# Kernel tuning notes

Measured on AMD Instinct MI355X. Metric: run time of the kernel, lower is better.

## Reference

```python
import jax, jax.numpy as jnp
import numpy as np
import math

B, T, C = 1, 4096, 1024
N_HEAD = 16
HEAD_DIM = C // N_HEAD


def _rotate_every_two(x):
    x1 = x[..., ::2]
    x2 = x[..., 1::2]
    return jnp.stack((-x2, x1), axis=-1).reshape(x.shape)


def setup_inputs() -> dict:
    key = jax.random.key(0)
    k1, k2, k3 = jax.random.split(key, 3)
    s = 0.02
    return {
        "x": jax.random.normal(k1, (B, T, C), dtype=jnp.float32),
        "Wqkv": jax.random.normal(k2, (C, 3 * C), dtype=jnp.float32) * s,
        "bqkv": jnp.zeros((3 * C,), dtype=jnp.float32),
        "Wproj": jax.random.normal(k3, (C, C), dtype=jnp.float32) * s,
        "bproj": jnp.zeros((C,), dtype=jnp.float32),
    }


def reference(x, Wqkv, bqkv, Wproj, bproj):
    b, t, c = x.shape
    qkv = x @ Wqkv + bqkv                      # [B,T,3C]
    q, k, v = jnp.split(qkv, 3, axis=2)
    # [B,H,T,D]
    q = q.reshape(b, t, N_HEAD, HEAD_DIM).transpose(0, 2, 1, 3)
    k = k.reshape(b, t, N_HEAD, HEAD_DIM).transpose(0, 2, 1, 3)
    v = v.reshape(b, t, N_HEAD, HEAD_DIM).transpose(0, 2, 1, 3)

    # RoPE (as in source: emb = cat(freqs, freqs), rotate_every_two interleaved)
    inv_freq = 1.0 / (10000.0 ** (jnp.arange(0, HEAD_DIM, 2, dtype=jnp.float32) / HEAD_DIM))
    pos = jnp.arange(t, dtype=jnp.float32)
    freqs = pos[:, None] * inv_freq[None, :]          # [T, D/2]
    emb = jnp.concatenate((freqs, freqs), axis=-1)    # [T, D]
    cos = jnp.cos(emb)[None, None, :, :]
    sin = jnp.sin(emb)[None, None, :, :]
    q = q * cos + _rotate_every_two(q) * sin
    k = k * cos + _rotate_every_two(k) * sin

    att = jnp.einsum('bhqd,bhkd->bhqk', q, k) / math.sqrt(HEAD_DIM)
    causal = jnp.tril(jnp.ones((t, t), dtype=bool))
    att = jnp.where(causal[None, None], att, -jnp.inf)
    att = jax.nn.softmax(att, axis=-1)
    y = jnp.einsum('bhqk,bhkd->bhqd', att, v)         # [B,H,T,D]
    y = y.transpose(0, 2, 1, 3).reshape(b, t, c)
    return y @ Wproj + bproj
```

## Files before the change

### kernel.cpp

```cpp
#include <hip/hip_runtime.h>
#include <hip/hip_bf16.h>
#include <cstdint>
#include <cstddef>

constexpr int TSEQ = 4096;
constexpr int CDIM = 1024;
constexpr int NHEAD = 16;
constexpr int HDIM = 64;
constexpr float QSCALE = 0.125f * 1.4426950408889634f;

using bf16 = __hip_bfloat16;
typedef __bf16 bf16x8 __attribute__((ext_vector_type(8)));
typedef float floatx4 __attribute__((ext_vector_type(4)));

__device__ inline uint32_t cvt_pk_bf16(float a, float b) {
  uint32_t r;
  asm("v_cvt_pk_bf16_f32 %0, %1, %2" : "=v"(r) : "v"(a), "v"(b));
  return r;
}
__device__ inline floatx4 vadd4(floatx4 a, floatx4 b) {
  floatx4 r;
  r[0] = a[0] + b[0]; r[1] = a[1] + b[1];
  r[2] = a[2] + b[2]; r[3] = a[3] + b[3];
  return r;
}

__global__ __launch_bounds__(256) void f32_to_bf16(
    const float4* __restrict__ in, uint64_t* __restrict__ out, int n4) {
  const int i = blockIdx.x * 256 + threadIdx.x;
  if (i < n4) {
    const float4 v = in[i];
    union { bf16 h[4]; uint64_t u; } p;
    p.h[0] = __float2bfloat16(v.x);
    p.h[1] = __float2bfloat16(v.y);
    p.h[2] = __float2bfloat16(v.z);
    p.h[3] = __float2bfloat16(v.w);
    out[i] = p.u;
  }
}

__global__ __launch_bounds__(256) void rope_table(float* __restrict__ tab) {
  const int i = blockIdx.x * 256 + threadIdx.x;
  const int t = i >> 5, j = i & 31;
  const float invf = exp2f((float)j * (-2.0f / 64.0f) * 13.287712379549449f);
  float sn, cs;
  sincosf((float)t * invf, &sn, &cs);
  tab[t * 64 + j] = cs;
  tab[t * 64 + 32 + j] = sn;
}

__global__ __launch_bounds__(256) void transpose_f32_bf16(
    const float* __restrict__ in, bf16* __restrict__ out, int R, int C) {
  __shared__ float tile[32][33];
  const int c0 = blockIdx.x * 32, r0 = blockIdx.y * 32;
  const int tx = threadIdx.x, ty = threadIdx.y;
#pragma unroll
  for (int i = 0; i < 32; i += 8)
    tile[ty + i][tx] = in[(size_t)(r0 + ty + i) * C + c0 + tx];
  __syncthreads();
#pragma unroll
  for (int i = 0; i < 32; i += 8)
    out[(size_t)(c0 + ty + i) * R + r0 + tx] = __float2bfloat16(tile[tx][ty + i]);
}

template <int MODE>
__global__ __launch_bounds__(256) void gemm_bt(
    const bf16* __restrict__ A, const bf16* __restrict__ Bt,
    const float* __restrict__ bias, const float* __restrict__ tab,
    float* __restrict__ Cout,
    bf16* __restrict__ Qh, bf16* __restrict__ Kh, bf16* __restrict__ Vt,
    int M, int N, int K) {
  __shared__ __align__(16) bf16 smem[4 * 64 * 72];
  bf16* As = smem;
  bf16* Bs = smem + 128 * 40;
  const int tid = threadIdx.x;
  const int m0 = blockIdx.y * 128, n0 = blockIdx.x * 128;
  const int wave = tid >> 6, lane = tid & 63;
  const int l15 = lane & 15, quad = lane >> 4;
  const int wm = (wave >> 1) * 64, wn = (wave & 1) * 64;

  const floatx4 fzero = {0.f, 0.f, 0.f, 0.f};
  floatx4 acc[4][4];
#pragma unroll
  for (int mi = 0; mi < 4; mi++)
#pragma unroll
    for (int ni = 0; ni < 4; ni++) acc[mi][ni] = fzero;

  const int row0 = tid >> 2;
  const int colb = (tid & 3) << 3;

  for (int k0 = 0; k0 < K; k0 += 32) {
    __syncthreads();
    *(float4*)(As + row0 * 40 + colb) =
        *(const float4*)(A + (size_t)(m0 + row0) * K + k0 + colb);
    *(float4*)(As + (row0 + 64) * 40 + colb) =
        *(const float4*)(A + (size_t)(m0 + row0 + 64) * K + k0 + colb);
    *(float4*)(Bs + row0 * 40 + colb) =
        *(const float4*)(Bt + (size_t)(n0 + row0) * K + k0 + colb);
    *(float4*)(Bs + (row0 + 64) * 40 + colb) =
        *(const float4*)(Bt + (size_t)(n0 + row0 + 64) * K + k0 + colb);
    __syncthreads();

    bf16x8 a[4], b[4];
#pragma unroll
    for (int mi = 0; mi < 4; mi++)
      a[mi] = *(const bf16x8*)(As + (wm + mi * 16 + l15) * 40 + quad * 8);
#pragma unroll
    for (int ni = 0; ni < 4; ni++)
      b[ni] = *(const bf16x8*)(Bs + (wn + ni * 16 + l15) * 40 + quad * 8);
#pragma unroll
    for (int mi = 0; mi < 4; mi++)
#pragma unroll
      for (int ni = 0; ni < 4; ni++)
        acc[mi][ni] = __builtin_amdgcn_mfma_f32_16x16x32_bf16(
            a[mi], b[ni], acc[mi][ni], 0, 0, 0);
  }

  __syncthreads();

  if (MODE == 1) {
    bf16* ep = smem + (size_t)wave * (64 * 72);
    const int cbase = n0 + wn;
    const int sec = cbase >> 10;
    const int hh = (cbase & 1023) >> 6;
    if (sec == 2) {
#pragma unroll
      for (int ni = 0; ni < 4; ni++) {
        const int d = ni * 16 + l15;
        const float bv = bias[cbase + d];
#pragma unroll
        for (int mi = 0; mi < 4; mi++) {
          const uint32_t lo =
              cvt_pk_bf16(acc[mi][ni][0] + bv, acc[mi][ni][1] + bv);
          const uint32_t hi =
              cvt_pk_bf16(acc[mi][ni][2] + bv, acc[mi][ni][3] + bv);
          *(uint64_t*)(ep + (size_t)d * 72 + mi * 16 + quad * 4) =
              (uint64_t)lo | ((uint64_t)hi << 32);
        }
      }
      __asm__ __volatile__("" ::: "memory");
#pragma unroll
      for (int it = 0; it < 8; it++) {
        const int dr = it * 8 + (lane >> 3);
        const int t8 = (lane & 7) * 8;
        const bf16x8 vv = *(const bf16x8*)(ep + (size_t)dr * 72 + t8);
        *(bf16x8*)(Vt + ((size_t)hh * HDIM + dr) * TSEQ + m0 + wm + t8) = vv;
      }
    } else {
      bf16* dst = (sec == 0) ? Qh : Kh;
      const float postscale = (sec == 0) ? QSCALE : 1.0f;
#pragma unroll
      for (int ni = 0; ni < 4; ni++) {
        const int c = ni * 16 + l15;
        const float bv = bias[cbase + c];
        const int j = c & 31;
#pragma unroll
        for (int mi = 0; mi < 4; mi++) {
#pragma unroll
          for (int r = 0; r < 4; r++) {
            const int t = m0 + wm + mi * 16 + quad * 4 + r;
            const float v = acc[mi][ni][r] + bv;
            const float partner = __shfl_xor(v, 1, 64);
            const float cs = tab[t * 64 + j];
            const float sn = tab[t * 64 + 32 + j];
            const float res =
                (v * cs + ((c & 1) ? partner : -partner) * sn) * postscale;
            ep[(size_t)(mi * 16 + quad * 4 + r) * 72 + c] =
                __float2bfloat16(res);
          }
        }
      }
      __asm__ __volatile__("" ::: "memory");
#pragma unroll
      for (int it = 0; it < 8; it++) {
        const int row = it * 8 + (lane >> 3);
        const int c8 = (lane & 7) * 8;
        const bf16x8 vv = *(const bf16x8*)(ep + (size_t)row * 72 + c8);
        *(bf16x8*)(dst + ((size_t)hh * TSEQ + m0 + wm + row) * HDIM + c8) = vv;
      }
    }
  } else {
    float* ep32 = (float*)smem + (size_t)wave * (32 * 68);
    float bvv[4];
#pragma unroll
    for (int ni = 0; ni < 4; ni++) bvv[ni] = bias[n0 + wn + ni * 16 + l15];
#pragma unroll
    for (int half = 0; half < 2; half++) {
      if (half) __asm__ __volatile__("" ::: "memory");
#pragma unroll
      for (int ni = 0; ni < 4; ni++)
#pragma unroll
        for (int mi2 = 0; mi2 < 2; mi2++)
#pragma unroll
          for (int r = 0; r < 4; r++)
            ep32[(size_t)(mi2 * 16 + quad * 4 + r) * 68 + ni * 16 + l15] =
                acc[half * 2 + mi2][ni][r] + bvv[ni];
      __asm__ __volatile__("" ::: "memory");
#pragma unroll
      for (int it = 0; it < 8; it++) {
        const int row = it * 4 + (lane >> 4);
        const float4 vv = *(const float4*)(ep32 + (size_t)row * 68 + l15 * 4);
        *(float4*)(Cout + (size_t)(m0 + wm + half * 32 + row) * N + n0 + wn +
                   l15 * 4) = vv;
      }
    }
  }
}

__global__ __launch_bounds__(256) void attn_kernel(
    const bf16* __restrict__ Qh, const bf16* __restrict__ Kh,
    const bf16* __restrict__ Vt, bf16* __restrict__ Y) {
  const int h = blockIdx.y;
  const int p = blockIdx.x;
  const int tile_lo = p, tile_hi = 63 - p;
  const int tid = threadIdx.x;
  const int w = tid >> 6, lane = tid & 63;
  const int l15 = lane & 15, quad = lane >> 4;
  const int q_lo = tile_lo * 64 + w * 16 + l15;
  const int q_hi = tile_hi * 64 + w * 16 + l15;
  const int nkv_lo = tile_lo + 1;
  const int nkv_hi = tile_hi + 1;

  const bf16* Qb = Qh + (size_t)h * TSEQ * HDIM;
  const bf16* Kb = Kh + (size_t)h * TSEQ * HDIM;
  const bf16* Vb = Vt + (size_t)h * HDIM * TSEQ;

  __shared__ __align__(16) bf16 Ks[2][64 * 64];
  __shared__ __align__(16) bf16 Vs[2][64 * 64];
  __shared__ bf16 Plds[4][32][72];

  const int sr = tid >> 3;
  const int sc = tid & 7;
  const int sp = sc << 3;
  const int sofs = sr * 64 + ((sc ^ (sr & 7)) << 3);

  bf16x8 Rk0, Rk1, Rv0, Rv1;
  auto stage_load = [&](int kv0) {
    Rk0 = *(const bf16x8*)(Kb + (size_t)(kv0 + sr) * HDIM + sp);
    Rk1 = *(const bf16x8*)(Kb + (size_t)(kv0 + sr + 32) * HDIM + sp);
    Rv0 = *(const bf16x8*)(Vb + (size_t)sr * TSEQ + kv0 + sp);
    Rv1 = *(const bf16x8*)(Vb + (size_t)(sr + 32) * TSEQ + kv0 + sp);
  };
  auto stage_write = [&](int buf) {
    *(bf16x8*)(Ks[buf] + sofs) = Rk0;
    *(bf16x8*)(Ks[buf] + sofs + 32 * 64) = Rk1;
    *(bf16x8*)(Vs[buf] + sofs) = Rv0;
    *(bf16x8*)(Vs[buf] + sofs + 32 * 64) = Rv1;
  };

  const int x7 = l15 & 7;
  const int fofs0 = ((quad ^ x7) << 3);
  const int fofs1 = (((4 + quad) ^ x7) << 3);

  bf16x8 qf[2][2];
#pragma unroll
  for (int ks = 0; ks < 2; ks++) {
    qf[0][ks] = *(const bf16x8*)(Qb + (size_t)q_lo * HDIM + ks * 32 + quad * 8);
    qf[1][ks] = *(const bf16x8*)(Qb + (size_t)q_hi * HDIM + ks * 32 + quad * 8);
  }

  const floatx4 fzero = {0.f, 0.f, 0.f, 0.f};
  floatx4 o[2][4];
  floatx4 lacc[2] = {fzero, fzero};
#pragma unroll
  for (int qt = 0; qt < 2; qt++)
#pragma unroll
    for (int dt = 0; dt < 4; dt++) o[qt][dt] = fzero;

  auto exp_tile = [&](floatx4* s, int qrow, bool maskit, int kv0, int qt) {
    if (maskit) {
#pragma unroll
      for (int kt = 0; kt < 4; kt++)
#pragma unroll
        for (int r = 0; r < 4; r++) {
          const int kv = kv0 + kt * 16 + quad * 4 + r;
          if (kv > qrow) s[kt][r] = -1e30f;
        }
    }
#pragma unroll
    for (int kt = 0; kt < 4; kt++)
#pragma unroll
      for (int r = 0; r < 4; r++)
        s[kt][r] = __builtin_amdgcn_exp2f(s[kt][r]);
    lacc[qt] = vadd4(lacc[qt], vadd4(vadd4(s[0], s[1]), vadd4(s[2], s[3])));
#pragma unroll
    for (int kt = 0; kt < 4; kt++) {
      const uint32_t lo = cvt_pk_bf16(s[kt][0], s[kt][1]);
      const uint32_t hi = cvt_pk_bf16(s[kt][2], s[kt][3]);
      *(uint64_t*)(&Plds[w][qt * 16 + l15][kt * 16 + quad * 4]) =
          (uint64_t)lo | ((uint64_t)hi << 32);
    }
  };

  stage_load(0);
  stage_write(0);
  __syncthreads();

  int cur = 0;
  for (int kb = 0; kb < nkv_hi; kb++) {
    const int kv0 = kb * 64;
    const bool lo_on = (kb < nkv_lo);
    const bool have_next = (kb + 1 < nkv_hi);

    if (have_next) stage_load(kv0 + 64);

    floatx4 sh[4], sl[4];
#pragma unroll
    for (int kt = 0; kt < 4; kt++) { sh[kt] = fzero; sl[kt] = fzero; }
    __builtin_amdgcn_s_setprio(1);
#pragma unroll
    for (int kt = 0; kt < 4; kt++) {
      const bf16* krow = Ks[cur] + (kt * 16 + l15) * 64;
      const bf16x8 kf0 = *(const bf16x8*)(krow + fofs0);
      const bf16x8 kf1 = *(const bf16x8*)(krow + fofs1);
      sh[kt] = __builtin_amdgcn_mfma_f32_16x16x32_bf16(
          kf0, qf[1][0], sh[kt], 0, 0, 0);
      sh[kt] = __builtin_amdgcn_mfma_f32_16x16x32_bf16(
          kf1, qf[1][1], sh[kt], 0, 0, 0);
      if (lo_on) {
        sl[kt] = __builtin_amdgcn_mfma_f32_16x16x32_bf16(
            kf0, qf[0][0], sl[kt], 0, 0, 0);
        sl[kt] = __builtin_amdgcn_mfma_f32_16x16x32_bf16(
            kf1, qf[0][1], sl[kt], 0, 0, 0);
      }
    }
    __builtin_amdgcn_s_setprio(0);

    exp_tile(sh, q_hi, kb == nkv_hi - 1, kv0, 1);
    if (lo_on) exp_tile(sl, q_lo, kb == nkv_lo - 1, kv0, 0);
    __asm__ __volatile__("" ::: "memory");

    bf16x8 ph[2], pl[2];
#pragma unroll
    for (int ks = 0; ks < 2; ks++)
      ph[ks] = *(const bf16x8*)(&Plds[w][16 + l15][ks * 32 + quad * 8]);
    if (lo_on) {
#pragma unroll
      for (int ks = 0; ks < 2; ks++)
        pl[ks] = *(const bf16x8*)(&Plds[w][l15][ks * 32 + quad * 8]);
    }
    __builtin_amdgcn_s_setprio(1);
#pragma unroll
    for (int dt = 0; dt < 4; dt++) {
      const bf16* vrow = Vs[cur] + (dt * 16 + l15) * 64;
      const bf16x8 vf0 = *(const bf16x8*)(vrow + fofs0);
      const bf16x8 vf1 = *(const bf16x8*)(vrow + fofs1);
      o[1][dt] = __builtin_amdgcn_mfma_f32_16x16x32_bf16(
          vf0, ph[0], o[1][dt], 0, 0, 0);
      o[1][dt] = __builtin_amdgcn_mfma_f32_16x16x32_bf16(
          vf1, ph[1], o[1][dt], 0, 0, 0);
      if (lo_on) {
        o[0][dt] = __builtin_amdgcn_mfma_f32_16x16x32_bf16(
            vf0, pl[0], o[0][dt], 0, 0, 0);
        o[0][dt] = __builtin_amdgcn_mfma_f32_16x16x32_bf16(
            vf1, pl[1], o[0][dt], 0, 0, 0);
      }
    }
    __builtin_amdgcn_s_setprio(0);

    if (have_next) stage_write(cur ^ 1);
    __syncthreads();
    cur ^= 1;
  }

#pragma unroll
  for (int qt = 0; qt < 2; qt++) {
    const int q = (qt == 0) ? q_lo : q_hi;
    float l = (lacc[qt][0] + lacc[qt][1]) + (lacc[qt][2] + lacc[qt][3]);
    l += __shfl_xor(l, 16, 64);
    l += __shfl_xor(l, 32, 64);
    const float inv = 1.0f / l;
#pragma unroll
    for (int dt = 0; dt < 4; dt++) {
      const uint32_t lo = cvt_pk_bf16(o[qt][dt][0] * inv, o[qt][dt][1] * inv);
      const uint32_t hi = cvt_pk_bf16(o[qt][dt][2] * inv, o[qt][dt][3] * inv);
      *(uint64_t*)(Y + (size_t)q * CDIM + h * HDIM + dt * 16 + quad * 4) =
          (uint64_t)lo | ((uint64_t)hi << 32);
    }
  }
}

extern "C" void kernel_launch(void* const* d_in, const int* in_sizes, int n_in,
                              void* d_out, int out_size, void* d_ws,
                              size_t ws_size, hipStream_t stream) {
  const float* x     = (const float*)d_in[0];
  const float* Wqkv  = (const float*)d_in[1];
  const float* bqkv  = (const float*)d_in[2];
  const float* Wproj = (const float*)d_in[3];
  const float* bproj = (const float*)d_in[4];
  float* out = (float*)d_out;

  char* ws = (char*)d_ws;
  bf16* xb     = (bf16*)(ws);
  bf16* Y      = (bf16*)(ws);
  bf16* WqkvT  = (bf16*)(ws + (8ull  << 20));
  bf16* WprojT = (bf16*)(ws + (14ull << 20));
  float* tab   = (float*)(ws + (14ull << 20));
  bf16* Qh     = (bf16*)(ws + (16ull << 20));
  bf16* Kh     = (bf16*)(ws + (24ull << 20));
  bf16* Vt     = (bf16*)(ws + (32ull << 20));

  f32_to_bf16<<<dim3(4096), 256, 0, stream>>>((const float4*)x, (uint64_t*)xb,
                                              TSEQ * CDIM / 4);
  transpose_f32_bf16<<<dim3(96, 32), dim3(32, 8), 0, stream>>>(
      Wqkv, WqkvT, CDIM, 3 * CDIM);
  rope_table<<<dim3(TSEQ * 32 / 256), 256, 0, stream>>>(tab);
  gemm_bt<1><<<dim3(24, 32), 256, 0, stream>>>(
      xb, WqkvT, bqkv, tab, (float*)nullptr, Qh, Kh, Vt, TSEQ, 3 * CDIM, CDIM);
  transpose_f32_bf16<<<dim3(32, 32), dim3(32, 8), 0, stream>>>(
      Wproj, WprojT, CDIM, CDIM);
  attn_kernel<<<dim3(32, 16), 256, 0, stream>>>(Qh, Kh, Vt, Y);
  gemm_bt<0><<<dim3(8, 32), 256, 0, stream>>>(
      Y, WprojT, bproj, (float*)nullptr, out, (bf16*)nullptr, (bf16*)nullptr,
      (bf16*)nullptr, TSEQ, CDIM, CDIM);
}
```

Baseline: 262.4 us.

## Load GEMM tiles directly to LDS with XOR swizzle and K-step 64

Replaces register-staged global-to-LDS copies in the GEMM main loop with direct global_load_lds 16-byte transfers. The K tile doubles from 32 to 64, and the padded LDS layout becomes an XOR-swizzled 64-wide layout so fragment reads avoid bank conflicts. The aim is to cut VGPR traffic and halve the number of barrier pairs per K. It still has no double buffering, so global latency remains exposed at each sync.

```diff
diff --git a/kernel.cpp b/kernel.cpp
--- a/kernel.cpp
+++ b/kernel.cpp
@@ -23,6 +23,11 @@
   r[0] = a[0] + b[0]; r[1] = a[1] + b[1];
   r[2] = a[2] + b[2]; r[3] = a[3] + b[3];
   return r;
+}
+__device__ inline void gload_lds16(const bf16* g, bf16* l) {
+  __builtin_amdgcn_global_load_lds(
+      (const __attribute__((address_space(1))) void*)g,
+      (__attribute__((address_space(3))) void*)l, 16, 0, 0);
 }
 
 __global__ __launch_bounds__(256) void f32_to_bf16(
@@ -72,7 +77,7 @@
     int M, int N, int K) {
   __shared__ __align__(16) bf16 smem[4 * 64 * 72];
   bf16* As = smem;
-  bf16* Bs = smem + 128 * 40;
+  bf16* Bs = smem + 128 * 64;
   const int tid = threadIdx.x;
   const int m0 = blockIdx.y * 128, n0 = blockIdx.x * 128;
   const int wave = tid >> 6, lane = tid & 63;
@@ -86,34 +91,47 @@
 #pragma unroll
     for (int ni = 0; ni < 4; ni++) acc[mi][ni] = fzero;
 
-  const int row0 = tid >> 2;
-  const int colb = (tid & 3) << 3;
-
-  for (int k0 = 0; k0 < K; k0 += 32) {
+  const int gr = lane >> 3;
+  const int gcs = ((lane & 7) ^ gr) << 3;
+  const bf16* Ag = A + (size_t)(m0 + wave * 32 + gr) * K + gcs;
+  const bf16* Bg = Bt + (size_t)(n0 + wave * 32 + gr) * K + gcs;
+  bf16* Asw = As + wave * 32 * 64;
+  bf16* Bsw = Bs + wave * 32 * 64;
+
+  const int x7f = l15 & 7;
+  const int af0 = (quad ^ x7f) << 3;
+  const int af1 = ((4 + quad) ^ x7f) << 3;
+
+  for (int k0 = 0; k0 < K; k0 += 64) {
     __syncthreads();
-    *(float4*)(As + row0 * 40 + colb) =
-        *(const float4*)(A + (size_t)(m0 + row0) * K + k0 + colb);
-    *(float4*)(As + (row0 + 64) * 40 + colb) =
-        *(const float4*)(A + (size_t)(m0 + row0 + 64) * K + k0 + colb);
-    *(float4*)(Bs + row0 * 40 + colb) =
-        *(const float4*)(Bt + (size_t)(n0 + row0) * K + k0 + colb);
-    *(float4*)(Bs + (row0 + 64) * 40 + colb) =
-        *(const float4*)(Bt + (size_t)(n0 + row0 + 64) * K + k0 + colb);
+#pragma unroll
+    for (int j = 0; j < 4; j++) {
+      gload_lds16(Ag + (size_t)j * 8 * K + k0, Asw + j * 512);
+      gload_lds16(Bg + (size_t)j * 8 * K + k0, Bsw + j * 512);
+    }
     __syncthreads();
 
-    bf16x8 a[4], b[4];
-#pragma unroll
-    for (int mi = 0; mi < 4; mi++)
-      a[mi] = *(const bf16x8*)(As + (wm + mi * 16 + l15) * 40 + quad * 8);
-#pragma unroll
-    for (int ni = 0; ni < 4; ni++)
-      b[ni] = *(const bf16x8*)(Bs + (wn + ni * 16 + l15) * 40 + quad * 8);
-#pragma unroll
-    for (int mi = 0; mi < 4; mi++)
-#pragma unroll
-      for (int ni = 0; ni < 4; ni++)
-        acc[mi][ni] = __builtin_amdgcn_mfma_f32_16x16x32_bf16(
-            a[mi], b[ni], acc[mi][ni], 0, 0, 0);
+    bf16x8 a[4][2], b[4][2];
+#pragma unroll
+    for (int mi = 0; mi < 4; mi++) {
+      const bf16* ar = As + (wm + mi * 16 + l15) * 64;
+      a[mi][0] = *(const bf16x8*)(ar + af0);
+      a[mi][1] = *(const bf16x8*)(ar + af1);
+    }
+#pragma unroll
+    for (int ni = 0; ni < 4; ni++) {
+      const bf16* br = Bs + (wn + ni * 16 + l15) * 64;
+      b[ni][0] = *(const bf16x8*)(br + af0);
+      b[ni][1] = *(const bf16x8*)(br + af1);
+    }
+#pragma unroll
+    for (int kk = 0; kk < 2; kk++)
+#pragma unroll
+      for (int mi = 0; mi < 4; mi++)
+#pragma unroll
+        for (int ni = 0; ni < 4; ni++)
+          acc[mi][ni] = __builtin_amdgcn_mfma_f32_16x16x32_bf16(
+              a[mi][kk], b[ni][kk], acc[mi][ni], 0, 0, 0);
   }
 
   __syncthreads();
```

Result: faster. 247.0 us (-5.9%).
